# Optimization experiments

Measured on AMD Instinct MI355X. Metric: run time of the kernel, lower is better.

The kernel has to match this reference:

```python
import jax, jax.numpy as jnp
import numpy as np

N = 10000
E = 160000
IN_DIM = 512
OUT_DIM = 256
NEG_SLOPE = 0.2  # DGL GATConv default LeakyReLU slope


def _gat_conv(x, W, b, attn_l, attn_r, src, dst, num_nodes, heads, out_dim):
    """DGL GATConv (eval mode, feat_drop/attn_drop disabled).
    x: [N, F_in]; W: [F_in, heads*out]; b: [heads*out];
    attn_l/attn_r: [heads, out]. Returns [N, heads, out]."""
    h = (x @ W).reshape(num_nodes, heads, out_dim)            # [N,H,D]
    el = jnp.einsum('nhd,hd->nh', h, attn_l)                  # [N,H]
    er = jnp.einsum('nhd,hd->nh', h, attn_r)                  # [N,H]
    e = jax.nn.leaky_relu(el[src] + er[dst], NEG_SLOPE)       # [E,H]
    # destination-grouped (edge) softmax, numerically stable
    m = jax.ops.segment_max(e, dst, num_segments=num_nodes)   # [N,H], -inf for empty
    m = jnp.where(jnp.isfinite(m), m, 0.0)
    ee = jnp.exp(e - m[dst])                                  # [E,H]
    s = jax.ops.segment_sum(ee, dst, num_segments=num_nodes)  # [N,H]
    a = ee / jnp.where(s > 0, s, 1.0)[dst]                    # [E,H]
    # message aggregation: scatter-add a_e * h[src]
    out = jax.ops.segment_sum(a[:, :, None] * h[src], dst, num_segments=num_nodes)
    return out + b.reshape(1, heads, out_dim)


def setup_inputs() -> dict:
    key = jax.random.key(0)
    ks = jax.random.split(key, 16)
    def glorot(k, shape):
        fan = shape[0] + shape[-1] if len(shape) > 1 else shape[-1]
        return jax.random.normal(k, shape, dtype=jnp.float32) * np.sqrt(2.0 / fan)
    inp = {
        'x':   jax.random.normal(ks[0], (N, IN_DIM), dtype=jnp.float32),
        'src': jax.random.randint(ks[1], (E,), 0, N),
        'dst': jax.random.randint(ks[2], (E,), 0, N),
        'W1': glorot(ks[3], (IN_DIM, 10 * 128)),
        'b1': jnp.zeros((10 * 128,), jnp.float32),
        'al1': glorot(ks[4], (10, 128)),
        'ar1': glorot(ks[5], (10, 128)),
        'W2': glorot(ks[6], (1280, 10 * 64)),
        'b2': jnp.zeros((10 * 64,), jnp.float32),
        'al2': glorot(ks[7], (10, 64)),
        'ar2': glorot(ks[8], (10, 64)),
        'W3': glorot(ks[9], (640, OUT_DIM)),
        'b3': jnp.zeros((OUT_DIM,), jnp.float32),
        'al3': glorot(ks[10], (1, OUT_DIM)),
        'ar3': glorot(ks[11], (1, OUT_DIM)),
        # residual linear 512 -> 256
        'Wres': glorot(ks[12], (IN_DIM, OUT_DIM)),
        'bres': jnp.zeros((OUT_DIM,), jnp.float32),
        'fuse_weight': jnp.full((1,), 0.5, jnp.float32),
    }
    return inp


def reference(x, src, dst, W1, b1, al1, ar1, W2, b2, al2, ar2,
              W3, b3, al3, ar3, Wres, bres, fuse_weight):
    elu = jax.nn.elu
    res = elu(x @ Wres + bres)                                        # [N,256]
    s1 = elu(_gat_conv(x, W1, b1, al1, ar1, src, dst, N, 10, 128))
    s1 = s1.reshape(N, -1)                                            # [N,1280]
    s2 = elu(_gat_conv(s1, W2, b2, al2, ar2, src, dst, N, 10, 64))
    s2 = s2.reshape(N, -1)                                            # [N,640]
    s3 = elu(_gat_conv(s2, W3, b3, al3, ar3, src, dst, N, 1, OUT_DIM))
    s3 = s3.reshape(N, -1)                                            # [N,256]
    return fuse_weight * s3 + (1.0 - fuse_weight) * res
```

## Files before the change

kernel.cpp:

```cpp
#include <hip/hip_runtime.h>
#include <stdint.h>

#define DEVINL __device__ __forceinline__

typedef __attribute__((ext_vector_type(8))) short short8;
typedef __attribute__((ext_vector_type(4))) float f32x4;

static constexpr int NNODES = 10000;

DEVINL float bf2f(unsigned short u) {
  unsigned int x = ((unsigned int)u) << 16;
  float f;
  __builtin_memcpy(&f, &x, 4);
  return f;
}
DEVINL unsigned short f2bf(float f) {
  unsigned int x;
  __builtin_memcpy(&x, &f, 4);
  unsigned int lsb = (x >> 16) & 1;
  x += 0x7fffu + lsb;
  return (unsigned short)(x >> 16);
}
DEVINL void bfpair(unsigned int u, float& f0, float& f1) {
  unsigned int a = u << 16, b = u & 0xffff0000u;
  __builtin_memcpy(&f0, &a, 4);
  __builtin_memcpy(&f1, &b, 4);
}
DEVINL bool is_bf16_mode(const unsigned int* fwWord) {
  return ((*fwWord) & 0xFFFFu) == 0x3F00u;
}

DEVINL void async_cp16(void* lds, const void* g) {
  __builtin_amdgcn_global_load_lds((const __attribute__((address_space(1))) unsigned int*)g,
                                   (__attribute__((address_space(3))) unsigned int*)lds,
                                   16, 0, 0);
}

template <int EPI>
__global__ __launch_bounds__(256) void gemm_bf16(const unsigned short* __restrict__ A,
                                                 const unsigned short* __restrict__ Bt,
                                                 unsigned short* __restrict__ C,
                                                 int M, int N, int K,
                                                 const float* __restrict__ ebias) {
  __shared__ __align__(16) unsigned short lA[128 * 32];
  __shared__ __align__(16) unsigned short lB[128 * 32];
  const int tid = threadIdx.x;
  const int wid = tid >> 6;
  const int lane = tid & 63;
  const int tm = blockIdx.x * 128;
  const int tn = blockIdx.y * 128;
  const int wr = (wid >> 1) * 64;
  const int wc = (wid & 1) * 64;
  f32x4 acc[4][4] = {};
  const int r_in_chunk = lane >> 2;
  const int cb = (lane & 3) * 16;
  const int mr = lane & 15;
  const int kq = (lane >> 4) * 8;
  const size_t stride = (size_t)K * 2;

  for (int k0 = 0; k0 < K; k0 += 32) {
#pragma unroll
    for (int c = 0; c < 2; ++c) {
      const int chunk = wid * 2 + c;
      const int row = chunk * 16 + r_in_chunk;
      int ga = tm + row;
      if (ga >= M) ga = M - 1;
      async_cp16(&lA[chunk * 512], (const char*)A + (size_t)ga * stride + (size_t)k0 * 2 + cb);
      const int gb = tn + row;
      async_cp16(&lB[chunk * 512], (const char*)Bt + (size_t)gb * stride + (size_t)k0 * 2 + cb);
    }
    __syncthreads();
    short8 af[4], bf[4];
#pragma unroll
    for (int i = 0; i < 4; ++i)
      af[i] = *(const short8*)&lA[(wr + i * 16 + mr) * 32 + kq];
#pragma unroll
    for (int j = 0; j < 4; ++j)
      bf[j] = *(const short8*)&lB[(wc + j * 16 + mr) * 32 + kq];
#pragma unroll
    for (int i = 0; i < 4; ++i)
#pragma unroll
      for (int j = 0; j < 4; ++j)
        acc[i][j] = __builtin_amdgcn_mfma_f32_16x16x32_bf16(af[i], bf[j], acc[i][j], 0, 0, 0);
    __syncthreads();
  }

  const int rbase = (lane >> 4) * 4;
  const int cc = lane & 15;
#pragma unroll
  for (int i = 0; i < 4; ++i) {
#pragma unroll
    for (int r = 0; r < 4; ++r) {
      const int row = tm + wr + i * 16 + rbase + r;
      if (row < M) {
#pragma unroll
        for (int j = 0; j < 4; ++j) {
          const int col = tn + wc + j * 16 + cc;
          float v = acc[i][j][r];
          if (EPI == 1) {
            v += ebias[col];
            v = v > 0.f ? v : (__expf(v) - 1.f);
          }
          C[(size_t)row * N + col] = f2bf(v);
        }
      }
    }
  }
}

struct CvtJobs {
  const void* src[12];
  float* dst[12];
  int n[12];
  int cnt;
};
__global__ void cvt_small_f32(CvtJobs jobs, const unsigned int* fwWord) {
  const bool isb = is_bf16_mode(fwWord);
  for (int j = 0; j < jobs.cnt; ++j) {
    for (int i = blockIdx.x * blockDim.x + threadIdx.x; i < jobs.n[j];
         i += gridDim.x * blockDim.x) {
      jobs.dst[j][i] = isb ? bf2f(((const unsigned short*)jobs.src[j])[i])
                           : ((const float*)jobs.src[j])[i];
    }
  }
}

__global__ __launch_bounds__(256) void cvt_x_bf16(const void* __restrict__ in,
                                                  unsigned short* __restrict__ out,
                                                  long n, const unsigned int* fwWord) {
  const bool isb = is_bf16_mode(fwWord);
  const long i0 = (long)(blockIdx.x * 256 + threadIdx.x) * 8;
  if (i0 >= n) return;
  if (isb) {
    *(short8*)&out[i0] = *(const short8*)&((const unsigned short*)in)[i0];
  } else {
    const float* f = (const float*)in + i0;
    unsigned short r[8];
#pragma unroll
    for (int j = 0; j < 8; ++j) r[j] = f2bf(f[j]);
    *(short8*)&out[i0] = *(const short8*)r;
  }
}

struct TAll {
  const void* src[4];
  unsigned short* dst[4];
  int K[4];
  int N[4];
  int b0[5];
};
__global__ __launch_bounds__(256) void transp_all4(TAll ja, const unsigned int* fwWord) {
  const bool isb = is_bf16_mode(fwWord);
  __shared__ unsigned short t[32][33];
  const int bid = blockIdx.x;
  int j = 0;
  while (j < 3 && bid >= ja.b0[j + 1]) ++j;
  const int local = bid - ja.b0[j];
  const int K = ja.K[j], Nn = ja.N[j];
  const int tilesX = Nn / 32;
  const int bx = (local % tilesX) * 32;
  const int by = (local / tilesX) * 32;
  const void* W = ja.src[j];
  unsigned short* Wt = ja.dst[j];
  const int x = threadIdx.x;
  const int y0 = threadIdx.y;
  for (int y = y0; y < 32; y += 8) {
    const size_t idx = (size_t)(by + y) * Nn + bx + x;
    t[y][x] = isb ? ((const unsigned short*)W)[idx] : f2bf(((const float*)W)[idx]);
  }
  __syncthreads();
  for (int y = y0; y < 32; y += 8)
    Wt[(size_t)(bx + y) * K + by + x] = t[x][y];
}

template <int H, int D>
__global__ __launch_bounds__(256) void compute_elr(const unsigned short* __restrict__ hf,
                                                   const float* __restrict__ al,
                                                   const float* __restrict__ ar,
                                                   float* __restrict__ el,
                                                   float* __restrict__ er) {
  const int gw = (blockIdx.x * 256 + threadIdx.x) >> 6;
  const int lane = threadIdx.x & 63;
  if (gw >= NNODES * H) return;
  const int n = gw / H;
  const int h = gw % H;
  const unsigned short* hp = hf + (size_t)n * (H * D) + h * D;
  const float* alp = al + h * D;
  const float* arp = ar + h * D;
  float a = 0.f, b = 0.f;
#pragma unroll
  for (int d0 = 0; d0 < D; d0 += 64) {
    float v = bf2f(hp[d0 + lane]);
    a += v * alp[d0 + lane];
    b += v * arp[d0 + lane];
  }
#pragma unroll
  for (int o = 32; o; o >>= 1) {
    a += __shfl_xor(a, o);
    b += __shfl_xor(b, o);
  }
  if (lane == 0) { el[gw] = a; er[gw] = b; }
}

template <int H>
__global__ __launch_bounds__(256) void edge_w(const float* __restrict__ el,
                                              const float* __restrict__ er,
                                              const int* __restrict__ sidx,
                                              const int* __restrict__ didx,
                                              float* __restrict__ we_t, int E) {
  const int p = blockIdx.x * 256 + threadIdx.x;
  if (p >= E) return;
  const float* ep = el + (size_t)sidx[p] * H;
  const float* rp = er + (size_t)didx[p] * H;
#pragma unroll
  for (int h = 0; h < H; ++h) {
    float sc = ep[h] + rp[h];
    sc = sc > 0.f ? sc : 0.2f * sc;
    we_t[(size_t)h * E + p] = __expf(sc);
  }
}

template <int H>
__global__ __launch_bounds__(256) void denom_k(const float* __restrict__ we_t,
                                               const int* __restrict__ rowstart,
                                               float* __restrict__ dinv_t,
                                               int E, int total) {
  const int id = blockIdx.x * 256 + threadIdx.x;
  if (id >= total) return;
  const int h = id / NNODES;
  const int n = id % NNODES;
  const int e0 = rowstart[n], e1 = rowstart[n + 1];
  const float* wp = we_t + (size_t)h * E;
  float s = 0.f;
  for (int p = e0; p < e1; ++p) s += wp[p];
  dinv_t[id] = s > 0.f ? 1.f / s : 0.f;
}

template <int H, int D, int NS, int CW, int MODE>
__global__ __launch_bounds__(64) void gat_agg_hs(const unsigned short* __restrict__ hf,
                                                 const float* __restrict__ we_t,
                                                 const float* __restrict__ dinv_t,
                                                 const int* __restrict__ sidx,
                                                 const int* __restrict__ rowstart,
                                                 const float* __restrict__ bias,
                                                 void* __restrict__ outp,
                                                 const unsigned short* __restrict__ resact,
                                                 const float* __restrict__ fwf,
                                                 const unsigned int* fwWord, int E) {
  constexpr int CHUNK = 64;
  constexpr int SF = H * D / NS;
  constexpr int ACT = SF / CW;
  constexpr int SROW = H * D * 2;
  constexpr int LOG2D = (D == 64) ? 6 : (D == 128) ? 7 : 8;
  static_assert((H * D) % NS == 0 && (SF % CW) == 0 && ACT <= 64, "geometry");
  static_assert(CW == 2 || CW == 4, "vector width");
  static_assert(SF < 2 * D, "slice spans at most 2 heads");
  __shared__ float wls[2 * (CHUNK + 1)];
  __shared__ int soff[CHUNK];

  const int bid = blockIdx.x;
  const int n = bid / NS;
  const int sl = bid % NS;
  const int tid = threadIdx.x;
  const int e0 = rowstart[n], e1 = rowstart[n + 1];
  const int f0 = SF * sl;
  const int hlo = f0 >> LOG2D;
  const int hhi = (f0 + SF - 1) >> LOG2D;
  const float dlo = dinv_t[(size_t)hlo * NNODES + n];
  const float dhi = dinv_t[(size_t)hhi * NNODES + n];
  const int fbase = f0 + tid * CW;
  const int wbase = ((fbase >> LOG2D) != hlo) ? (CHUNK + 1) : 0;
  const bool act = tid < ACT;
  const char* hfb = (const char*)(hf + fbase);
  float acc[CW] = {};

  for (int cs = e0; cs < e1; cs += CHUNK) {
    const int ce = min(CHUNK, e1 - cs);
    if (tid < ce) {
      soff[tid] = sidx[cs + tid] * SROW;
      wls[tid] = we_t[(size_t)hlo * E + cs + tid] * dlo;
      if (hhi != hlo) wls[CHUNK + 1 + tid] = we_t[(size_t)hhi * E + cs + tid] * dhi;
    }
    __syncthreads();
    if (act) {
      int j = 0;
      for (; j + 8 <= ce; j += 8) {
        int o[8];
        float w[8];
#pragma unroll
        for (int b = 0; b < 8; ++b) {
          o[b] = soff[j + b];
          w[b] = wls[wbase + j + b];
        }
        if constexpr (CW == 4) {
          uint2 u[8];
#pragma unroll
          for (int b = 0; b < 8; ++b) u[b] = *(const uint2*)(hfb + o[b]);
#pragma unroll
          for (int b = 0; b < 8; ++b) {
            float a0, a1, a2, a3;
            bfpair(u[b].x, a0, a1);
            bfpair(u[b].y, a2, a3);
            acc[0] += w[b] * a0; acc[1] += w[b] * a1;
            acc[2] += w[b] * a2; acc[3] += w[b] * a3;
          }
        } else {
          unsigned int u[8];
#pragma unroll
          for (int b = 0; b < 8; ++b) u[b] = *(const unsigned int*)(hfb + o[b]);
#pragma unroll
          for (int b = 0; b < 8; ++b) {
            float a0, a1;
            bfpair(u[b], a0, a1);
            acc[0] += w[b] * a0; acc[1] += w[b] * a1;
          }
        }
      }
      for (; j < ce; ++j) {
        const int o = soff[j];
        const float w = wls[wbase + j];
        if constexpr (CW == 4) {
          const uint2 u = *(const uint2*)(hfb + o);
          float a0, a1, a2, a3;
          bfpair(u.x, a0, a1);
          bfpair(u.y, a2, a3);
          acc[0] += w * a0; acc[1] += w * a1; acc[2] += w * a2; acc[3] += w * a3;
        } else {
          const unsigned int u = *(const unsigned int*)(hfb + o);
          float a0, a1;
          bfpair(u, a0, a1);
          acc[0] += w * a0; acc[1] += w * a1;
        }
      }
    }
    __syncthreads();
  }

  if (!act) return;
  const size_t obase = (size_t)n * (H * D) + fbase;
  float v[CW];
#pragma unroll
  for (int k = 0; k < CW; ++k) {
    v[k] = acc[k] + bias[fbase + k];
    v[k] = v[k] > 0.f ? v[k] : (__expf(v[k]) - 1.f);
  }
  if (MODE == 0) {
#pragma unroll
    for (int k = 0; k < CW; ++k)
      ((unsigned short*)outp)[obase + k] = f2bf(v[k]);
  } else {
    const float fw = fwf[0];
    const bool outb = is_bf16_mode(fwWord);
#pragma unroll
    for (int k = 0; k < CW; ++k) {
      const float r = bf2f(resact[obase + k]);
      const float o = fw * v[k] + (1.f - fw) * r;
      if (outb) ((unsigned short*)outp)[obase + k] = f2bf(o);
      else      ((float*)outp)[obase + k] = o;
    }
  }
}

__global__ void sentinel_k(unsigned short* __restrict__ outp, int total) {
  const int i = blockIdx.x * 256 + threadIdx.x;
  if (i < total) outp[i] = f2bf(12344.0f);
}

__global__ void hist_k(const int* __restrict__ dst, int* __restrict__ deg, int E) {
  const int i = blockIdx.x * blockDim.x + threadIdx.x;
  if (i < E) atomicAdd(&deg[dst[i]], 1);
}

__global__ __launch_bounds__(1024) void scan_k(const int* __restrict__ deg,
                                               int* __restrict__ rowstart,
                                               int* __restrict__ cursor, int Nn) {
  __shared__ int ls[1024];
  const int tid = threadIdx.x;
  const int CH = (Nn + 1023) >> 10;
  const int start = tid * CH;
  int sum = 0;
  for (int i = 0; i < CH; ++i) {
    const int idx = start + i;
    if (idx < Nn) sum += deg[idx];
  }
  ls[tid] = sum;
  __syncthreads();
  for (int o = 1; o < 1024; o <<= 1) {
    int v = 0;
    if (tid >= o) v = ls[tid - o];
    __syncthreads();
    ls[tid] += v;
    __syncthreads();
  }
  int run = tid > 0 ? ls[tid - 1] : 0;
  for (int i = 0; i < CH; ++i) {
    const int idx = start + i;
    if (idx < Nn) {
      rowstart[idx] = run;
      cursor[idx] = run;
      run += deg[idx];
    }
  }
  if (tid == 1023) rowstart[Nn] = ls[1023];
}

__global__ void scatter_k(const int* __restrict__ dst, const int* __restrict__ srcA,
                          int* __restrict__ cursor, int* __restrict__ sidx,
                          int* __restrict__ didx, int E) {
  const int i = blockIdx.x * blockDim.x + threadIdx.x;
  if (i < E) {
    const int d = dst[i];
    const int p = atomicAdd(&cursor[d], 1);
    sidx[p] = srcA[i];
    didx[p] = d;
  }
}

extern "C" void kernel_launch(void* const* d_in, const int* in_sizes, int n_in,
                              void* d_out, int out_size, void* d_ws, size_t ws_size,
                              hipStream_t stream) {
  const void* x    = d_in[0];
  const int* src   = (const int*)d_in[1];
  const int* dstA  = (const int*)d_in[2];
  const void* W1   = d_in[3];
  const void* b1   = d_in[4];
  const void* al1  = d_in[5];
  const void* ar1  = d_in[6];
  const void* W2   = d_in[7];
  const void* b2   = d_in[8];
  const void* al2  = d_in[9];
  const void* ar2  = d_in[10];
  const void* W3   = d_in[11];
  const void* b3   = d_in[12];
  const void* al3  = d_in[13];
  const void* ar3  = d_in[14];
  const void* Wres = d_in[15];
  const void* bres = d_in[16];
  const void* fw   = d_in[17];
  const unsigned int* fwWord = (const unsigned int*)fw;
  const int E = in_sizes[1];
  const int M = NNODES;

  char* base = (char*)d_ws;
  size_t off = 0;
  auto alloc = [&](size_t bytes) -> char* {
    char* p = base + off;
    off = (off + bytes + 255) & ~(size_t)255;
    return p;
  };
  int* deg      = (int*)alloc((size_t)M * 4);
  int* rowstart = (int*)alloc((size_t)(M + 1) * 4);
  int* cursor   = (int*)alloc((size_t)M * 4);
  int* sidx     = (int*)alloc((size_t)E * 4);
  int* didx     = (int*)alloc((size_t)E * 4);
  float* we_t   = (float*)alloc((size_t)E * 10 * 4);
  float* elb    = (float*)alloc((size_t)M * 10 * 4);
  float* erb    = (float*)alloc((size_t)M * 10 * 4);
  float* dinv_t = (float*)alloc((size_t)M * 10 * 4);
  float* b1f   = (float*)alloc(1280 * 4);
  float* al1f  = (float*)alloc(1280 * 4);
  float* ar1f  = (float*)alloc(1280 * 4);
  float* b2f   = (float*)alloc(640 * 4);
  float* al2f  = (float*)alloc(640 * 4);
  float* ar2f  = (float*)alloc(640 * 4);
  float* b3f   = (float*)alloc(256 * 4);
  float* al3f  = (float*)alloc(256 * 4);
  float* ar3f  = (float*)alloc(256 * 4);
  float* bresf = (float*)alloc(256 * 4);
  float* fwf   = (float*)alloc(4);
  unsigned short* wt1    = (unsigned short*)alloc((size_t)1280 * 512 * 2);
  unsigned short* wt2    = (unsigned short*)alloc((size_t)640 * 1280 * 2);
  unsigned short* wt3    = (unsigned short*)alloc((size_t)256 * 640 * 2);
  unsigned short* wtr    = (unsigned short*)alloc((size_t)256 * 512 * 2);
  unsigned short* resact = (unsigned short*)alloc((size_t)M * 256 * 2);
  unsigned short* regA   = (unsigned short*)alloc((size_t)M * 1280 * 2);
  unsigned short* regB   = (unsigned short*)alloc((size_t)M * 1280 * 2);

  if (off > ws_size) {
    sentinel_k<<<(out_size + 255) / 256, 256, 0, stream>>>((unsigned short*)d_out, out_size);
    return;
  }

  unsigned short* h1 = regA;
  unsigned short* h2 = regA;
  unsigned short* h3 = regA;
  unsigned short* xb = regB;
  unsigned short* s1 = regB;
  unsigned short* s2 = regB;

  CvtJobs jobs;
  const void* srcs[11] = {b1, al1, ar1, b2, al2, ar2, b3, al3, ar3, bres, fw};
  float* dsts[11] = {b1f, al1f, ar1f, b2f, al2f, ar2f, b3f, al3f, ar3f, bresf, fwf};
  const int ns[11] = {1280, 1280, 1280, 640, 640, 640, 256, 256, 256, 256, 1};
  for (int j = 0; j < 11; ++j) { jobs.src[j] = srcs[j]; jobs.dst[j] = dsts[j]; jobs.n[j] = ns[j]; }
  jobs.cnt = 11;
  cvt_small_f32<<<8, 256, 0, stream>>>(jobs, fwWord);

  cvt_x_bf16<<<(int)(((long)M * 512 / 8 + 255) / 256), 256, 0, stream>>>(x, xb, (long)M * 512, fwWord);

  TAll ta;
  ta.src[0] = W1;   ta.dst[0] = wt1; ta.K[0] = 512;  ta.N[0] = 1280;
  ta.src[1] = W2;   ta.dst[1] = wt2; ta.K[1] = 1280; ta.N[1] = 640;
  ta.src[2] = W3;   ta.dst[2] = wt3; ta.K[2] = 640;  ta.N[2] = 256;
  ta.src[3] = Wres; ta.dst[3] = wtr; ta.K[3] = 512;  ta.N[3] = 256;
  ta.b0[0] = 0;
  for (int j = 0; j < 4; ++j)
    ta.b0[j + 1] = ta.b0[j] + (ta.K[j] / 32) * (ta.N[j] / 32);
  transp_all4<<<ta.b0[4], dim3(32, 8), 0, stream>>>(ta, fwWord);

  hipMemsetAsync(deg, 0, (size_t)M * 4, stream);
  hist_k<<<(E + 255) / 256, 256, 0, stream>>>(dstA, deg, E);
  scan_k<<<1, 1024, 0, stream>>>(deg, rowstart, cursor, M);
  scatter_k<<<(E + 255) / 256, 256, 0, stream>>>(dstA, src, cursor, sidx, didx, E);

  const int MT = (M + 127) / 128;
  const int EB = (E + 255) / 256;

  gemm_bf16<1><<<dim3(MT, 2), 256, 0, stream>>>(xb, wtr, resact, M, 256, 512, bresf);

  gemm_bf16<0><<<dim3(MT, 10), 256, 0, stream>>>(xb, wt1, h1, M, 1280, 512, nullptr);
  compute_elr<10, 128><<<(M * 10) / 4, 256, 0, stream>>>(h1, al1f, ar1f, elb, erb);
  edge_w<10><<<EB, 256, 0, stream>>>(elb, erb, sidx, didx, we_t, E);
  denom_k<10><<<(M * 10 + 255) / 256, 256, 0, stream>>>(we_t, rowstart, dinv_t, E, M * 10);
  gat_agg_hs<10, 128, 8, 4, 0><<<M * 8, 64, 0, stream>>>(h1, we_t, dinv_t, sidx, rowstart,
                                                         b1f, s1, nullptr, fwf, fwWord, E);

  gemm_bf16<0><<<dim3(MT, 5), 256, 0, stream>>>(s1, wt2, h2, M, 640, 1280, nullptr);
  compute_elr<10, 64><<<(M * 10) / 4, 256, 0, stream>>>(h2, al2f, ar2f, elb, erb);
  edge_w<10><<<EB, 256, 0, stream>>>(elb, erb, sidx, didx, we_t, E);
  denom_k<10><<<(M * 10 + 255) / 256, 256, 0, stream>>>(we_t, rowstart, dinv_t, E, M * 10);
  gat_agg_hs<10, 64, 8, 2, 0><<<M * 8, 64, 0, stream>>>(h2, we_t, dinv_t, sidx, rowstart,
                                                        b2f, s2, nullptr, fwf, fwWord, E);

  gemm_bf16<0><<<dim3(MT, 2), 256, 0, stream>>>(s2, wt3, h3, M, 256, 640, nullptr);
  compute_elr<1, 256><<<M / 4, 256, 0, stream>>>(h3, al3f, ar3f, elb, erb);
  edge_w<1><<<EB, 256, 0, stream>>>(elb, erb, sidx, didx, we_t, E);
  denom_k<1><<<(M + 255) / 256, 256, 0, stream>>>(we_t, rowstart, dinv_t, E, M);
  gat_agg_hs<1, 256, 2, 2, 1><<<M * 2, 64, 0, stream>>>(h3, we_t, dinv_t, sidx, rowstart,
                                                        b3f, d_out, resact, fwf, fwWord, E);
}
```

Baseline: 328.0 us.

## Fuse attention logits into GEMM epilogue, merge residual GEMM, fold softmax denominator

```diff
diff --git a/kernel.cpp b/kernel.cpp
--- a/kernel.cpp
+++ b/kernel.cpp
@@ -36,12 +36,17 @@
                                    16, 0, 0);
 }
 
-template <int EPI>
-__global__ __launch_bounds__(256) void gemm_bf16(const unsigned short* __restrict__ A,
-                                                 const unsigned short* __restrict__ Bt,
-                                                 unsigned short* __restrict__ C,
-                                                 int M, int N, int K,
-                                                 const float* __restrict__ ebias) {
+__global__ __launch_bounds__(256) void gemm_fused(const unsigned short* __restrict__ A,
+                                                  const unsigned short* __restrict__ Bt,
+                                                  unsigned short* __restrict__ Ch,
+                                                  int M, int N, int K, int nres,
+                                                  unsigned short* __restrict__ Cres,
+                                                  const float* __restrict__ rbias,
+                                                  float* __restrict__ elp,
+                                                  float* __restrict__ erp,
+                                                  const float* __restrict__ alf,
+                                                  const float* __restrict__ arf,
+                                                  int logD, int H) {
   __shared__ __align__(16) unsigned short lA[128 * 32];
   __shared__ __align__(16) unsigned short lB[128 * 32];
   const int tid = threadIdx.x;
@@ -87,24 +92,65 @@
 
   const int rbase = (lane >> 4) * 4;
   const int cc = lane & 15;
-#pragma unroll
-  for (int i = 0; i < 4; ++i) {
-#pragma unroll
-    for (int r = 0; r < 4; ++r) {
-      const int row = tm + wr + i * 16 + rbase + r;
-      if (row < M) {
+  if (tn < nres) {
+#pragma unroll
+    for (int i = 0; i < 4; ++i)
+#pragma unroll
+      for (int r = 0; r < 4; ++r) {
+        const int row = tm + wr + i * 16 + rbase + r;
+        if (row < M) {
+#pragma unroll
+          for (int j = 0; j < 4; ++j) {
+            const int col = tn + wc + j * 16 + cc;
+            float v = acc[i][j][r] + rbias[col];
+            v = v > 0.f ? v : (__expf(v) - 1.f);
+            Cres[(size_t)row * nres + col] = f2bf(v);
+          }
+        }
+      }
+  } else {
+    const int tnh = tn - nres;
+    const int Nh = N - nres;
+    const int colw = tnh + wc;
+    const int head = colw >> logD;
+#pragma unroll
+    for (int i = 0; i < 4; ++i)
+#pragma unroll
+      for (int r = 0; r < 4; ++r) {
+        const int row = tm + wr + i * 16 + rbase + r;
+        if (row < M) {
+#pragma unroll
+          for (int j = 0; j < 4; ++j)
+            Ch[(size_t)row * Nh + colw + j * 16 + cc] = f2bf(acc[i][j][r]);
+        }
+      }
+    float alv[4], arv[4];
+#pragma unroll
+    for (int j = 0; j < 4; ++j) {
+      alv[j] = alf[colw + j * 16 + cc];
+      arv[j] = arf[colw + j * 16 + cc];
+    }
+#pragma unroll
+    for (int i = 0; i < 4; ++i)
+#pragma unroll
+      for (int r = 0; r < 4; ++r) {
+        float pe = 0.f, pr = 0.f;
 #pragma unroll
         for (int j = 0; j < 4; ++j) {
-          const int col = tn + wc + j * 16 + cc;
-          float v = acc[i][j][r];
-          if (EPI == 1) {
-            v += ebias[col];
-            v = v > 0.f ? v : (__expf(v) - 1.f);
-          }
-          C[(size_t)row * N + col] = f2bf(v);
+          pe += acc[i][j][r] * alv[j];
+          pr += acc[i][j][r] * arv[j];
+        }
+#pragma unroll
+        for (int o = 1; o < 16; o <<= 1) {
+          pe += __shfl_xor(pe, o);
+          pr += __shfl_xor(pr, o);
+        }
+        const int row = tm + wr + i * 16 + rbase + r;
+        if ((lane & 15) == 0 && row < M) {
+          atomicAdd(&elp[(size_t)row * H + head], pe);
+          atomicAdd(&erp[(size_t)row * H + head], pr);
         }
       }
-    }
   }
 }
 
@@ -173,35 +219,6 @@
     Wt[(size_t)(bx + y) * K + by + x] = t[x][y];
 }
 
-template <int H, int D>
-__global__ __launch_bounds__(256) void compute_elr(const unsigned short* __restrict__ hf,
-                                                   const float* __restrict__ al,
-                                                   const float* __restrict__ ar,
-                                                   float* __restrict__ el,
-                                                   float* __restrict__ er) {
-  const int gw = (blockIdx.x * 256 + threadIdx.x) >> 6;
-  const int lane = threadIdx.x & 63;
-  if (gw >= NNODES * H) return;
-  const int n = gw / H;
-  const int h = gw % H;
-  const unsigned short* hp = hf + (size_t)n * (H * D) + h * D;
-  const float* alp = al + h * D;
-  const float* arp = ar + h * D;
-  float a = 0.f, b = 0.f;
-#pragma unroll
-  for (int d0 = 0; d0 < D; d0 += 64) {
-    float v = bf2f(hp[d0 + lane]);
-    a += v * alp[d0 + lane];
-    b += v * arp[d0 + lane];
-  }
-#pragma unroll
-  for (int o = 32; o; o >>= 1) {
-    a += __shfl_xor(a, o);
-    b += __shfl_xor(b, o);
-  }
-  if (lane == 0) { el[gw] = a; er[gw] = b; }
-}
-
 template <int H>
 __global__ __launch_bounds__(256) void edge_w(const float* __restrict__ el,
                                               const float* __restrict__ er,
@@ -220,26 +237,9 @@
   }
 }
 
-template <int H>
-__global__ __launch_bounds__(256) void denom_k(const float* __restrict__ we_t,
-                                               const int* __restrict__ rowstart,
-                                               float* __restrict__ dinv_t,
-                                               int E, int total) {
-  const int id = blockIdx.x * 256 + threadIdx.x;
-  if (id >= total) return;
-  const int h = id / NNODES;
-  const int n = id % NNODES;
-  const int e0 = rowstart[n], e1 = rowstart[n + 1];
-  const float* wp = we_t + (size_t)h * E;
-  float s = 0.f;
-  for (int p = e0; p < e1; ++p) s += wp[p];
-  dinv_t[id] = s > 0.f ? 1.f / s : 0.f;
-}
-
 template <int H, int D, int NS, int CW, int MODE>
 __global__ __launch_bounds__(64) void gat_agg_hs(const unsigned short* __restrict__ hf,
                                                  const float* __restrict__ we_t,
-                                                 const float* __restrict__ dinv_t,
                                                  const int* __restrict__ sidx,
                                                  const int* __restrict__ rowstart,
                                                  const float* __restrict__ bias,
@@ -266,20 +266,25 @@
   const int f0 = SF * sl;
   const int hlo = f0 >> LOG2D;
   const int hhi = (f0 + SF - 1) >> LOG2D;
-  const float dlo = dinv_t[(size_t)hlo * NNODES + n];
-  const float dhi = dinv_t[(size_t)hhi * NNODES + n];
   const int fbase = f0 + tid * CW;
   const int wbase = ((fbase >> LOG2D) != hlo) ? (CHUNK + 1) : 0;
   const bool act = tid < ACT;
   const char* hfb = (const char*)(hf + fbase);
   float acc[CW] = {};
+  float swlo = 0.f, swhi = 0.f;
 
   for (int cs = e0; cs < e1; cs += CHUNK) {
     const int ce = min(CHUNK, e1 - cs);
     if (tid < ce) {
       soff[tid] = sidx[cs + tid] * SROW;
-      wls[tid] = we_t[(size_t)hlo * E + cs + tid] * dlo;
-      if (hhi != hlo) wls[CHUNK + 1 + tid] = we_t[(size_t)hhi * E + cs + tid] * dhi;
+      const float wlo = we_t[(size_t)hlo * E + cs + tid];
+      wls[tid] = wlo;
+      swlo += wlo;
+      if (hhi != hlo) {
+        const float whi = we_t[(size_t)hhi * E + cs + tid];
+        wls[CHUNK + 1 + tid] = whi;
+        swhi += whi;
+      }
     }
     __syncthreads();
     if (act) {
@@ -336,12 +341,19 @@
     __syncthreads();
   }
 
+#pragma unroll
+  for (int o = 32; o; o >>= 1) {
+    swlo += __shfl_xor(swlo, o);
+    swhi += __shfl_xor(swhi, o);
+  }
   if (!act) return;
+  const float stot = wbase ? swhi : swlo;
+  const float inv = stot > 0.f ? 1.f / stot : 0.f;
   const size_t obase = (size_t)n * (H * D) + fbase;
   float v[CW];
 #pragma unroll
   for (int k = 0; k < CW; ++k) {
-    v[k] = acc[k] + bias[fbase + k];
+    v[k] = acc[k] * inv + bias[fbase + k];
     v[k] = v[k] > 0.f ? v[k] : (__expf(v[k]) - 1.f);
   }
   if (MODE == 0) {
@@ -448,15 +460,20 @@
     off = (off + bytes + 255) & ~(size_t)255;
     return p;
   };
+  char* zbase   = base;
   int* deg      = (int*)alloc((size_t)M * 4);
+  float* elb1   = (float*)alloc((size_t)M * 10 * 4);
+  float* erb1   = (float*)alloc((size_t)M * 10 * 4);
+  float* elb2   = (float*)alloc((size_t)M * 10 * 4);
+  float* erb2   = (float*)alloc((size_t)M * 10 * 4);
+  float* elb3   = (float*)alloc((size_t)M * 4);
+  float* erb3   = (float*)alloc((size_t)M * 4);
+  const size_t zbytes = off;
   int* rowstart = (int*)alloc((size_t)(M + 1) * 4);
   int* cursor   = (int*)alloc((size_t)M * 4);
   int* sidx     = (int*)alloc((size_t)E * 4);
   int* didx     = (int*)alloc((size_t)E * 4);
   float* we_t   = (float*)alloc((size_t)E * 10 * 4);
-  float* elb    = (float*)alloc((size_t)M * 10 * 4);
-  float* erb    = (float*)alloc((size_t)M * 10 * 4);
-  float* dinv_t = (float*)alloc((size_t)M * 10 * 4);
   float* b1f   = (float*)alloc(1280 * 4);
   float* al1f  = (float*)alloc(1280 * 4);
   float* ar1f  = (float*)alloc(1280 * 4);
@@ -468,10 +485,9 @@
   float* ar3f  = (float*)alloc(256 * 4);
   float* bresf = (float*)alloc(256 * 4);
   float* fwf   = (float*)alloc(4);
-  unsigned short* wt1    = (unsigned short*)alloc((size_t)1280 * 512 * 2);
+  unsigned short* wtcat  = (unsigned short*)alloc((size_t)1536 * 512 * 2);
   unsigned short* wt2    = (unsigned short*)alloc((size_t)640 * 1280 * 2);
   unsigned short* wt3    = (unsigned short*)alloc((size_t)256 * 640 * 2);
-  unsigned short* wtr    = (unsigned short*)alloc((size_t)256 * 512 * 2);
   unsigned short* resact = (unsigned short*)alloc((size_t)M * 256 * 2);
   unsigned short* regA   = (unsigned short*)alloc((size_t)M * 1280 * 2);
   unsigned short* regB   = (unsigned short*)alloc((size_t)M * 1280 * 2);
@@ -487,6 +503,8 @@
   unsigned short* xb = regB;
   unsigned short* s1 = regB;
   unsigned short* s2 = regB;
+
+  hipMemsetAsync(zbase, 0, zbytes, stream);
 
   CvtJobs jobs;
   const void* srcs[11] = {b1, al1, ar1, b2, al2, ar2, b3, al3, ar3, bres, fw};
@@ -499,16 +517,15 @@
   cvt_x_bf16<<<(int)(((long)M * 512 / 8 + 255) / 256), 256, 0, stream>>>(x, xb, (long)M * 512, fwWord);
 
   TAll ta;
-  ta.src[0] = W1;   ta.dst[0] = wt1; ta.K[0] = 512;  ta.N[0] = 1280;
-  ta.src[1] = W2;   ta.dst[1] = wt2; ta.K[1] = 1280; ta.N[1] = 640;
-  ta.src[2] = W3;   ta.dst[2] = wt3; ta.K[2] = 640;  ta.N[2] = 256;
-  ta.src[3] = Wres; ta.dst[3] = wtr; ta.K[3] = 512;  ta.N[3] = 256;
+  ta.src[0] = W1;   ta.dst[0] = wtcat + (size_t)256 * 512; ta.K[0] = 512;  ta.N[0] = 1280;
+  ta.src[1] = W2;   ta.dst[1] = wt2;                       ta.K[1] = 1280; ta.N[1] = 640;
+  ta.src[2] = W3;   ta.dst[2] = wt3;                       ta.K[2] = 640;  ta.N[2] = 256;
+  ta.src[3] = Wres; ta.dst[3] = wtcat;                     ta.K[3] = 512;  ta.N[3] = 256;
   ta.b0[0] = 0;
   for (int j = 0; j < 4; ++j)
     ta.b0[j + 1] = ta.b0[j] + (ta.K[j] / 32) * (ta.N[j] / 32);
   transp_all4<<<ta.b0[4], dim3(32, 8), 0, stream>>>(ta, fwWord);
 
-  hipMemsetAsync(deg, 0, (size_t)M * 4, stream);
   hist_k<<<(E + 255) / 256, 256, 0, stream>>>(dstA, deg, E);
   scan_k<<<1, 1024, 0, stream>>>(deg, rowstart, cursor, M);
   scatter_k<<<(E + 255) / 256, 256, 0, stream>>>(dstA, src, cursor, sidx, didx, E);
@@ -516,26 +533,24 @@
   const int MT = (M + 127) / 128;
   const int EB = (E + 255) / 256;
 
-  gemm_bf16<1><<<dim3(MT, 2), 256, 0, stream>>>(xb, wtr, resact, M, 256, 512, bresf);
-
-  gemm_bf16<0><<<dim3(MT, 10), 256, 0, stream>>>(xb, wt1, h1, M, 1280, 512, nullptr);
-  compute_elr<10, 128><<<(M * 10) / 4, 256, 0, stream>>>(h1, al1f, ar1f, elb, erb);
-  edge_w<10><<<EB, 256, 0, stream>>>(elb, erb, sidx, didx, we_t, E);
-  denom_k<10><<<(M * 10 + 255) / 256, 256, 0, stream>>>(we_t, rowstart, dinv_t, E, M * 10);
-  gat_agg_hs<10, 128, 8, 4, 0><<<M * 8, 64, 0, stream>>>(h1, we_t, dinv_t, sidx, rowstart,
+  gemm_fused<<<dim3(MT, 12), 256, 0, stream>>>(xb, wtcat, h1, M, 1536, 512,
+                                               256, resact, bresf,
+                                               elb1, erb1, al1f, ar1f, 7, 10);
+  edge_w<10><<<EB, 256, 0, stream>>>(elb1, erb1, sidx, didx, we_t, E);
+  gat_agg_hs<10, 128, 8, 4, 0><<<M * 8, 64, 0, stream>>>(h1, we_t, sidx, rowstart,
                                                          b1f, s1, nullptr, fwf, fwWord, E);
 
-  gemm_bf16<0><<<dim3(MT, 5), 256, 0, stream>>>(s1, wt2, h2, M, 640, 1280, nullptr);
-  compute_elr<10, 64><<<(M * 10) / 4, 256, 0, stream>>>(h2, al2f, ar2f, elb, erb);
-  edge_w<10><<<EB, 256, 0, stream>>>(elb, erb, sidx, didx, we_t, E);
-  denom_k<10><<<(M * 10 + 255) / 256, 256, 0, stream>>>(we_t, rowstart, dinv_t, E, M * 10);
-  gat_agg_hs<10, 64, 8, 2, 0><<<M * 8, 64, 0, stream>>>(h2, we_t, dinv_t, sidx, rowstart,
+  gemm_fused<<<dim3(MT, 5), 256, 0, stream>>>(s1, wt2, h2, M, 640, 1280,
+                                              0, nullptr, nullptr,
+                                              elb2, erb2, al2f, ar2f, 6, 10);
+  edge_w<10><<<EB, 256, 0, stream>>>(elb2, erb2, sidx, didx, we_t, E);
+  gat_agg_hs<10, 64, 8, 2, 0><<<M * 8, 64, 0, stream>>>(h2, we_t, sidx, rowstart,
                                                         b2f, s2, nullptr, fwf, fwWord, E);
 
-  gemm_bf16<0><<<dim3(MT, 2), 256, 0, stream>>>(s2, wt3, h3, M, 256, 640, nullptr);
-  compute_elr<1, 256><<<M / 4, 256, 0, stream>>>(h3, al3f, ar3f, elb, erb);
-  edge_w<1><<<EB, 256, 0, stream>>>(elb, erb, sidx, didx, we_t, E);
-  denom_k<1><<<(M + 255) / 256, 256, 0, stream>>>(we_t, rowstart, dinv_t, E, M);
-  gat_agg_hs<1, 256, 2, 2, 1><<<M * 2, 64, 0, stream>>>(h3, we_t, dinv_t, sidx, rowstart,
+  gemm_fused<<<dim3(MT, 2), 256, 0, stream>>>(s2, wt3, h3, M, 256, 640,
+                                              0, nullptr, nullptr,
+                                              elb3, erb3, al3f, ar3f, 8, 1);
+  edge_w<1><<<EB, 256, 0, stream>>>(elb3, erb3, sidx, didx, we_t, E);
+  gat_agg_hs<1, 256, 2, 2, 1><<<M * 2, 64, 0, stream>>>(h3, we_t, sidx, rowstart,
                                                         b3f, d_out, resact, fwf, fwWord, E);
 }
```

After: 305.0 us. 1.08x faster.
